# Kernel tuning notes

Measured on AMD Instinct MI355X. Metric: run time of the kernel, lower is better.

Reference implementation:

```python
import jax, jax.numpy as jnp
import numpy as np

N = 100000      # num_nodes
E = 1600000     # num_edges (avg degree 16)
D_IN = 128
D_H = 128
D_OUT = 128


def setup_inputs() -> dict:
    key = jax.random.key(0)
    ks = jax.random.split(key, 6)
    x = jax.random.normal(ks[0], (N, D_IN), dtype=jnp.float32)
    edge_index = jax.random.randint(ks[1], (2, E), 0, N, dtype=jnp.int32)
    s_in = 1.0 / np.sqrt(D_IN)
    s_h = 1.0 / np.sqrt(D_H)
    # nn.Linear weights have shape [out_features, in_features]
    w_neigh1 = jax.random.uniform(ks[2], (D_H, D_IN), jnp.float32, -s_in, s_in)
    w_root1 = jax.random.uniform(ks[3], (D_H, D_IN), jnp.float32, -s_in, s_in)
    w_neigh2 = jax.random.uniform(ks[4], (D_OUT, D_H), jnp.float32, -s_h, s_h)
    w_root2 = jax.random.uniform(ks[5], (D_OUT, D_H), jnp.float32, -s_h, s_h)
    return {
        "x": x,
        "w_neigh1": w_neigh1,
        "w_root1": w_root1,
        "w_neigh2": w_neigh2,
        "w_root2": w_root2,
        "edge_index": edge_index,
    }


def reference(x, w_neigh1, w_root1, w_neigh2, w_root2, edge_index):
    row = edge_index[0]  # destination (row of adjacency)
    col = edge_index[1]  # source / neighbor (column of adjacency)
    # row-normalized adjacency: adj[row, col] = 1 / deg(row)
    deg = jax.ops.segment_sum(jnp.ones(E, x.dtype), row, num_segments=N)
    inv_deg = jnp.where(deg > 0, 1.0 / jnp.maximum(deg, 1.0), 0.0)  # [N]

    def mean_agg(h):
        # spmm: gather neighbor feats [E, d], scatter-add to rows, normalize
        return jax.ops.segment_sum(h[col], row, num_segments=N) * inv_deg[:, None]

    # layer 0: relu(adj @ x @ Wn1^T + x @ Wr1^T)
    h = jax.nn.relu(mean_agg(x) @ w_neigh1.T + x @ w_root1.T)
    # layer 1: adj @ h @ Wn2^T + h @ Wr2^T
    return mean_agg(h) @ w_neigh2.T + h @ w_root2.T
```

## Files before the change

kernel.cpp:

```cpp
#include <hip/hip_runtime.h>

#define NBUK_MAX 2048
#define BNODE 64
#define SORT_CAP 1536
#define AGG_NODES 16
#define AGG_CAP 768
#define SUPER_SHIFT 11
#define NSUPER_MAX 64
#define SUB_PER_SUPER 32

#define QSCALE (127.0f / 6.0f)
#define DEQ (6.0f / 127.0f)

typedef __attribute__((ext_vector_type(8))) short bf16x8;
typedef __attribute__((ext_vector_type(4))) float f32x4;

static __device__ __forceinline__ unsigned int f2bf(float f) {
  unsigned int t = __builtin_bit_cast(unsigned int, f);
  t += 0x7fff + ((t >> 16) & 1);
  return t >> 16;
}
static __device__ __forceinline__ unsigned char f2q(float v) {
  float q = rintf(v * QSCALE);
  q = fminf(fmaxf(q, -127.f), 127.f);
  return (unsigned char)(signed char)(int)q;
}
static __device__ __forceinline__ int sb(unsigned int u, int k) {
  return (int)((signed char)(u >> (k * 8)));
}


__global__ __launch_bounds__(256) void prep_kernel(
    const float* __restrict__ x, unsigned short* __restrict__ Xb,
    unsigned char* __restrict__ Xq, const int* __restrict__ row,
    int* __restrict__ bcount, const float* __restrict__ wn1,
    const float* __restrict__ wr1, const float* __restrict__ wn2,
    const float* __restrict__ wr2, unsigned short* __restrict__ Wp, int N, int E,
    int nbuk, int cvtB) {
  __shared__ int h[NBUK_MAX];
  const int b = blockIdx.x;
  const int tid = threadIdx.x;
  if (b < cvtB) {
    int i = b * 256 + tid;
    int n4 = N * 32;
    if (i < n4) {
      float4 v = ((const float4*)x)[i];
      ushort4 ob;
      ob.x = (unsigned short)f2bf(v.x);
      ob.y = (unsigned short)f2bf(v.y);
      ob.z = (unsigned short)f2bf(v.z);
      ob.w = (unsigned short)f2bf(v.w);
      ((ushort4*)Xb)[i] = ob;
      unsigned int oq = (unsigned)f2q(v.x) | ((unsigned)f2q(v.y) << 8) |
                        ((unsigned)f2q(v.z) << 16) | ((unsigned)f2q(v.w) << 24);
      ((unsigned int*)Xq)[i] = oq;
    }
  } else if (b < cvtB + 256) {
    for (int i = tid; i < nbuk; i += 256) h[i] = 0;
    __syncthreads();
    int hb = b - cvtB;
    for (int e = hb * 256 + tid; e < E; e += 256 * 256)
      atomicAdd(&h[row[e] >> 6], 1);
    __syncthreads();
    for (int i = tid; i < nbuk; i += 256)
      if (h[i]) atomicAdd(&bcount[i], h[i]);
  } else {
    int i = (b - cvtB - 256) * 256 + tid;
    int layer = i >> 15;
    int r = i & 32767;
    int ks = r >> 12;
    int nf = (r >> 9) & 7;
    int lane = (r >> 3) & 63;
    int j = r & 7;
    const float* src = layer ? ((ks < 4) ? wn2 : wr2) : ((ks < 4) ? wn1 : wr1);
    int m = lane & 15, kgrp = lane >> 4;
    int kk = (ks & 3) * 32 + kgrp * 8 + j;
    int n = nf * 16 + m;
    Wp[i] = (unsigned short)f2bf(src[n * 128 + kk]);
  }
}


__global__ __launch_bounds__(1024) void bucket_scan_kernel(
    const int* __restrict__ bcount, int* __restrict__ boff,
    int* __restrict__ bfill, int* __restrict__ sfill, int nbuk, int nsuper,
    int E) {
  __shared__ int s[1024];
  int carry = 0;
  int t = threadIdx.x;
  for (int base = 0; base < nbuk; base += 1024) {
    int v = (base + t < nbuk) ? bcount[base + t] : 0;
    s[t] = v;
    __syncthreads();
    for (int off = 1; off < 1024; off <<= 1) {
      int u = (t >= off) ? s[t - off] : 0;
      __syncthreads();
      s[t] += u;
      __syncthreads();
    }
    if (base + t < nbuk) {
      int ex = carry + s[t] - v;
      boff[base + t] = ex;
      bfill[base + t] = ex;
    }
    carry += s[1023];
    __syncthreads();
  }
  if (t == 0) boff[nbuk] = E;
  __syncthreads();
  if (t < nsuper) {
    int b = t * SUB_PER_SUPER;
    sfill[t] = boff[b > nbuk ? nbuk : b];
  }
}


__global__ __launch_bounds__(256) void s1_scatter(
    const int* __restrict__ row, const int* __restrict__ col,
    int* __restrict__ sfill, int* __restrict__ sbuf, int E) {
  __shared__ int cnt[NSUPER_MAX];
  __shared__ int base[NSUPER_MAX];
  int per = (E + gridDim.x - 1) / gridDim.x;
  int e0 = blockIdx.x * per;
  int e1 = e0 + per;
  if (e1 > E) e1 = E;
  if (threadIdx.x < NSUPER_MAX) cnt[threadIdx.x] = 0;
  __syncthreads();
  for (int e = e0 + threadIdx.x; e < e1; e += 256)
    atomicAdd(&cnt[row[e] >> SUPER_SHIFT], 1);
  __syncthreads();
  if (threadIdx.x < NSUPER_MAX) {
    int c = cnt[threadIdx.x];
    base[threadIdx.x] = c ? atomicAdd(&sfill[threadIdx.x], c) : 0;
    cnt[threadIdx.x] = 0;
  }
  __syncthreads();
  for (int e = e0 + threadIdx.x; e < e1; e += 256) {
    int r = row[e];
    int sp = r >> SUPER_SHIFT;
    int rk = atomicAdd(&cnt[sp], 1);
    sbuf[base[sp] + rk] = ((r & ((1 << SUPER_SHIFT) - 1)) << 17) | col[e];
  }
}


__global__ __launch_bounds__(256) void s2_scatter(
    const int* __restrict__ boff, const int* __restrict__ sbuf,
    int* __restrict__ bfill, int* __restrict__ bbuf, int nbuk) {
  __shared__ int cnt[SUB_PER_SUPER];
  __shared__ int base[SUB_PER_SUPER];
  const int sp = blockIdx.x >> 4;
  const int bp = blockIdx.x & 15;
  const int b0 = sp * SUB_PER_SUPER;
  int bend = b0 + SUB_PER_SUPER;
  if (bend > nbuk) bend = nbuk;
  const int sstart = boff[b0];
  const int len = boff[bend] - sstart;
  const int i0 = sstart + (len * bp) / 16;
  const int i1 = sstart + (len * (bp + 1)) / 16;
  if (threadIdx.x < SUB_PER_SUPER) cnt[threadIdx.x] = 0;
  __syncthreads();
  for (int i = i0 + threadIdx.x; i < i1; i += 256)
    atomicAdd(&cnt[(((unsigned)sbuf[i]) >> 17) >> 6], 1);
  __syncthreads();
  if (threadIdx.x < SUB_PER_SUPER) {
    int c = cnt[threadIdx.x];
    base[threadIdx.x] = c ? atomicAdd(&bfill[b0 + threadIdx.x], c) : 0;
    cnt[threadIdx.x] = 0;
  }
  __syncthreads();
  for (int i = i0 + threadIdx.x; i < i1; i += 256) {
    int p = sbuf[i];
    unsigned rl = ((unsigned)p) >> 17;
    int sub = rl >> 6;
    int rk = atomicAdd(&cnt[sub], 1);
    bbuf[base[sub] + rk] = ((rl & 63) << 17) | (p & 0x1FFFF);
  }
}


__global__ __launch_bounds__(256) void p2_sort_kernel(
    const int* __restrict__ boff, int* __restrict__ bbuf,
    int* __restrict__ rowptr, int* __restrict__ ovf, int N, int E) {
  __shared__ int cols[SORT_CAP];
  __shared__ int hist[BNODE], startc[BNODE], fillc[BNODE];
  const int b = blockIdx.x;
  const int tid = threadIdx.x;
  const int gs = boff[b], ge = boff[b + 1];
  const int bsize = ge - gs;
  if (tid < BNODE) hist[tid] = 0;
  __syncthreads();
  for (int i = gs + tid; i < ge; i += 256)
    atomicAdd(&hist[((unsigned)bbuf[i]) >> 17], 1);
  __syncthreads();
  if (tid < 64) {
    int v = hist[tid];
    int s = v;
    #pragma unroll
    for (int off = 1; off < 64; off <<= 1) {
      int u = __shfl_up(s, off, 64);
      if (tid >= off) s += u;
    }
    startc[tid] = s - v;
    fillc[tid] = s - v;
  }
  __syncthreads();
  const bool fast = (bsize <= SORT_CAP);
  if (fast) {
    for (int i = tid; i < bsize; i += 256) {
      int p = bbuf[gs + i];
      int k = atomicAdd(&fillc[((unsigned)p) >> 17], 1);
      cols[k] = p & 0x1FFFF;
    }
  }
  __syncthreads();
  if (fast) {
    for (int i = tid; i < bsize; i += 256) bbuf[gs + i] = cols[i];
  } else if (tid == 0) {
    ovf[b] = 1;
  }
  if (tid < BNODE) {
    int node = b * BNODE + tid;
    if (node < N) rowptr[node] = gs + startc[tid];
  }
  if (b == 0 && tid == 0) rowptr[N] = E;
}


__global__ __launch_bounds__(256) void agg_i8_kernel(
    const unsigned char* __restrict__ qtab, const int* __restrict__ rowptr,
    const int* __restrict__ bbuf, const int* __restrict__ boff,
    const int* __restrict__ ovf, unsigned short* __restrict__ out, int N) {
  __shared__ int cols[AGG_CAP];
  __shared__ int rp[AGG_NODES + 1];
  const int tid = threadIdx.x;
  const int n0 = blockIdx.x * AGG_NODES;
  if (tid <= AGG_NODES) {
    int nn = n0 + tid;
    rp[tid] = rowptr[nn > N ? N : nn];
  }
  __syncthreads();
  const int e0 = rp[0];
  const int range = rp[AGG_NODES] - e0;
  const int buck = n0 >> 6;
  const bool bovf = (ovf[buck] != 0);
  const bool lds = (!bovf) && (range <= AGG_CAP);
  if (lds) {
    for (int i = tid; i < range; i += 256) cols[i] = bbuf[e0 + i];
  }
  __syncthreads();

  const int g = tid >> 4;
  const int fl = tid & 15;
  const int node = n0 + g;
  if (node >= N) return;
  const int d = rp[g + 1] - rp[g];
  const char* fb = (const char*)qtab;
  const unsigned foff = (unsigned)fl * 8;
  int a[8];
  #pragma unroll
  for (int j = 0; j < 8; ++j) a[j] = 0;

  if (!bovf) {
    const int* cp = lds ? (cols + (rp[g] - e0)) : (bbuf + rp[g]);
    int k = 0;
    for (; k + 8 <= d; k += 8) {
      unsigned o[8];
      #pragma unroll
      for (int j = 0; j < 8; ++j) o[j] = ((unsigned)cp[k + j] << 7) + foff;
      uint2 v[8];
      #pragma unroll
      for (int j = 0; j < 8; ++j) v[j] = *(const uint2*)(fb + o[j]);
      #pragma unroll
      for (int j = 0; j < 8; ++j) {
        a[0] += sb(v[j].x, 0);
        a[1] += sb(v[j].x, 1);
        a[2] += sb(v[j].x, 2);
        a[3] += sb(v[j].x, 3);
        a[4] += sb(v[j].y, 0);
        a[5] += sb(v[j].y, 1);
        a[6] += sb(v[j].y, 2);
        a[7] += sb(v[j].y, 3);
      }
    }
    for (; k < d; ++k) {
      uint2 v = *(const uint2*)(fb + (((unsigned)cp[k] << 7) + foff));
      a[0] += sb(v.x, 0);
      a[1] += sb(v.x, 1);
      a[2] += sb(v.x, 2);
      a[3] += sb(v.x, 3);
      a[4] += sb(v.y, 0);
      a[5] += sb(v.y, 1);
      a[6] += sb(v.y, 2);
      a[7] += sb(v.y, 3);
    }
  } else {
    int gsb = boff[buck], geb = boff[buck + 1];
    unsigned int nl = (unsigned)(node & (BNODE - 1));
    for (int i = gsb; i < geb; ++i) {
      int p = bbuf[i];
      if ((((unsigned)p) >> 17) == nl) {
        uint2 v = *(const uint2*)(fb + (((unsigned)(p & 0x1FFFF) << 7) + foff));
        a[0] += sb(v.x, 0);
        a[1] += sb(v.x, 1);
        a[2] += sb(v.x, 2);
        a[3] += sb(v.x, 3);
        a[4] += sb(v.y, 0);
        a[5] += sb(v.y, 1);
        a[6] += sb(v.y, 2);
        a[7] += sb(v.y, 3);
      }
    }
  }

  float m = ((d > 0) ? 1.0f / (float)d : 0.f) * DEQ;
  uint4 pk;
  pk.x = f2bf((float)a[0] * m) | (f2bf((float)a[1] * m) << 16);
  pk.y = f2bf((float)a[2] * m) | (f2bf((float)a[3] * m) << 16);
  pk.z = f2bf((float)a[4] * m) | (f2bf((float)a[5] * m) << 16);
  pk.w = f2bf((float)a[6] * m) | (f2bf((float)a[7] * m) << 16);
  *(uint4*)((char*)out + ((unsigned)node << 8) + (unsigned)fl * 16) = pk;
}


template <bool RELU, bool OUT_BF16, bool EMIT_I8>
__global__ __launch_bounds__(256) void mfma_gemm_kernel(
    const unsigned short* __restrict__ Aagg,
    const unsigned short* __restrict__ Aroot,
    const unsigned short* __restrict__ Wpack,
    void* __restrict__ Cout, unsigned char* __restrict__ Qout, int nrows) {
  const int lane = threadIdx.x & 63;
  const int wid = threadIdx.x >> 6;
  const int row0 = blockIdx.x * 64 + wid * 16;
  const int m = lane & 15;
  const int kgrp = lane >> 4;
  int arow = row0 + m;
  if (arow > nrows - 1) arow = nrows - 1;

  bf16x8 a[8];
  #pragma unroll
  for (int ks = 0; ks < 4; ++ks)
    a[ks] = *(const bf16x8*)(Aagg + (size_t)arow * 128 + ks * 32 + kgrp * 8);
  #pragma unroll
  for (int ks = 4; ks < 8; ++ks)
    a[ks] = *(const bf16x8*)(Aroot + (size_t)arow * 128 + (ks - 4) * 32 + kgrp * 8);

  f32x4 acc[8];
  #pragma unroll
  for (int i = 0; i < 8; ++i) acc[i] = (f32x4){0.f, 0.f, 0.f, 0.f};

  const unsigned short* wp = Wpack + (size_t)lane * 8;
  #pragma unroll
  for (int ks = 0; ks < 8; ++ks) {
    #pragma unroll
    for (int nf = 0; nf < 8; ++nf) {
      bf16x8 bfr = *(const bf16x8*)(wp + ((ks * 8 + nf) << 9));
      acc[nf] = __builtin_amdgcn_mfma_f32_16x16x32_bf16(a[ks], bfr, acc[nf], 0, 0, 0);
    }
  }

  const int crow0 = row0 + kgrp * 4;
  #pragma unroll
  for (int nf = 0; nf < 8; ++nf) {
    int c = nf * 16 + m;
    #pragma unroll
    for (int j = 0; j < 4; ++j) {
      int r = crow0 + j;
      if (r < nrows) {
        float v = acc[nf][j];
        if (RELU) v = fmaxf(v, 0.f);
        if (OUT_BF16)
          ((unsigned short*)Cout)[(size_t)r * 128 + c] = (unsigned short)f2bf(v);
        else
          ((float*)Cout)[(size_t)r * 128 + c] = v;
        if (EMIT_I8) Qout[(size_t)r * 128 + c] = f2q(v);
      }
    }
  }
}


extern "C" void kernel_launch(void* const* d_in, const int* in_sizes, int n_in,
                              void* d_out, int out_size, void* d_ws, size_t ws_size,
                              hipStream_t stream) {
  const float* x = (const float*)d_in[0];
  const float* wn1 = (const float*)d_in[1];
  const float* wr1 = (const float*)d_in[2];
  const float* wn2 = (const float*)d_in[3];
  const float* wr2 = (const float*)d_in[4];
  const int* ei = (const int*)d_in[5];
  const int N = in_sizes[0] / 128;
  const int E = in_sizes[5] / 2;
  const int* row = ei;
  const int* col = ei + E;
  const int NBUK = (N + BNODE - 1) / BNODE;
  const int NSUPER = (N + (1 << SUPER_SHIFT) - 1) >> SUPER_SHIFT;

  char* p = (char*)d_ws;
  unsigned short* Xb = (unsigned short*)p;  p += (size_t)N * 128 * 2;
  unsigned short* Hb = (unsigned short*)p;  p += (size_t)N * 128 * 2;
  int* bbuf = (int*)p;      p += (size_t)E * 4;
  int* sbuf = (int*)p;      p += (size_t)E * 4;
  int* rowptr = (int*)p;    p += (size_t)(N + 1) * 4;
  int* bcount = (int*)p;    p += NBUK_MAX * 4;
  int* ovf = (int*)p;       p += NBUK_MAX * 4;
  int* boff = (int*)p;      p += (NBUK_MAX + 1) * 4;
  int* bfill = (int*)p;     p += NBUK_MAX * 4;
  int* sfill = (int*)p;     p += NSUPER_MAX * 4;
  unsigned short* Wp = (unsigned short*)p;  p += 2 * 32768 * 2;
  unsigned short* Wp1 = Wp;
  unsigned short* Wp2 = Wp + 32768;

  unsigned short* agg1 = (unsigned short*)d_out;
  unsigned char* Xq = (unsigned char*)d_out + (size_t)N * 128 * 2;
  unsigned char* Hq = (unsigned char*)d_out + (size_t)N * 128 * 3;
  unsigned short* agg2 = Xb;

  hipMemsetAsync(bcount, 0, 2 * NBUK_MAX * 4, stream);
  int cvtB = (N * 32 + 255) / 256;
  prep_kernel<<<cvtB + 512, 256, 0, stream>>>(x, Xb, Xq, row, bcount, wn1, wr1,
                                              wn2, wr2, Wp, N, E, NBUK, cvtB);

  bucket_scan_kernel<<<1, 1024, 0, stream>>>(bcount, boff, bfill, sfill, NBUK,
                                             NSUPER, E);
  s1_scatter<<<512, 256, 0, stream>>>(row, col, sfill, sbuf, E);
  s2_scatter<<<NSUPER * 16, 256, 0, stream>>>(boff, sbuf, bfill, bbuf, NBUK);
  p2_sort_kernel<<<NBUK, 256, 0, stream>>>(boff, bbuf, rowptr, ovf, N, E);

  agg_i8_kernel<<<(N + AGG_NODES - 1) / AGG_NODES, 256, 0, stream>>>(
      Xq, rowptr, bbuf, boff, ovf, agg1, N);
  mfma_gemm_kernel<true, true, true><<<(N + 63) / 64, 256, 0, stream>>>(
      agg1, Xb, Wp1, Hb, Hq, N);

  agg_i8_kernel<<<(N + AGG_NODES - 1) / AGG_NODES, 256, 0, stream>>>(
      Hq, rowptr, bbuf, boff, ovf, agg2, N);
  mfma_gemm_kernel<false, false, false><<<(N + 63) / 64, 256, 0, stream>>>(
      agg2, Hb, Wp2, (void*)d_out, nullptr, N);
}
```

Before: 204.5 us.

## Fuse int8 neighbor aggregation with MFMA GEMM per 64-node bucket

Each layer now runs as one kernel. A block aggregates the int8 neighbor features for a 64-node bucket into an LDS tile, then runs the bf16 MFMA projection directly from that tile, so the aggregated matrix is never written to or read back from global memory. Layer 1 converts fp32 x to bf16 on the fly in the GEMM, which drops the separate bf16 copy of x from the prep kernel. The cost is fewer, heavier blocks in which each thread gathers for four nodes in sequence, so there is less parallelism to hide gather latency.

```diff
diff --git a/kernel.cpp b/kernel.cpp
--- a/kernel.cpp
+++ b/kernel.cpp
@@ -3,8 +3,6 @@
 #define NBUK_MAX 2048
 #define BNODE 64
 #define SORT_CAP 1536
-#define AGG_NODES 16
-#define AGG_CAP 768
 #define SUPER_SHIFT 11
 #define NSUPER_MAX 64
 #define SUB_PER_SUPER 32
@@ -31,12 +29,11 @@
 
 
 __global__ __launch_bounds__(256) void prep_kernel(
-    const float* __restrict__ x, unsigned short* __restrict__ Xb,
-    unsigned char* __restrict__ Xq, const int* __restrict__ row,
-    int* __restrict__ bcount, const float* __restrict__ wn1,
-    const float* __restrict__ wr1, const float* __restrict__ wn2,
-    const float* __restrict__ wr2, unsigned short* __restrict__ Wp, int N, int E,
-    int nbuk, int cvtB) {
+    const float* __restrict__ x, unsigned char* __restrict__ Xq,
+    const int* __restrict__ row, int* __restrict__ bcount,
+    const float* __restrict__ wn1, const float* __restrict__ wr1,
+    const float* __restrict__ wn2, const float* __restrict__ wr2,
+    unsigned short* __restrict__ Wp, int N, int E, int nbuk, int cvtB) {
   __shared__ int h[NBUK_MAX];
   const int b = blockIdx.x;
   const int tid = threadIdx.x;
@@ -45,12 +42,6 @@
     int n4 = N * 32;
     if (i < n4) {
       float4 v = ((const float4*)x)[i];
-      ushort4 ob;
-      ob.x = (unsigned short)f2bf(v.x);
-      ob.y = (unsigned short)f2bf(v.y);
-      ob.z = (unsigned short)f2bf(v.z);
-      ob.w = (unsigned short)f2bf(v.w);
-      ((ushort4*)Xb)[i] = ob;
       unsigned int oq = (unsigned)f2q(v.x) | ((unsigned)f2q(v.y) << 8) |
                         ((unsigned)f2q(v.z) << 16) | ((unsigned)f2q(v.w) << 24);
       ((unsigned int*)Xq)[i] = oq;
@@ -227,128 +218,152 @@
 }
 
 
-__global__ __launch_bounds__(256) void agg_i8_kernel(
-    const unsigned char* __restrict__ qtab, const int* __restrict__ rowptr,
-    const int* __restrict__ bbuf, const int* __restrict__ boff,
-    const int* __restrict__ ovf, unsigned short* __restrict__ out, int N) {
-  __shared__ int cols[AGG_CAP];
-  __shared__ int rp[AGG_NODES + 1];
+template <bool L1>
+__global__ __launch_bounds__(256) void fused_kernel(
+    const unsigned char* __restrict__ qtab,
+    const void* __restrict__ root,
+    const unsigned short* __restrict__ Wpack,
+    const int* __restrict__ rowptr, const int* __restrict__ bbuf,
+    const int* __restrict__ ovf, void* __restrict__ Cout,
+    unsigned char* __restrict__ Qout, int nrows) {
+  __shared__ short aggL[BNODE][132];
+  __shared__ int cols[SORT_CAP];
+  __shared__ int rp[BNODE + 1];
   const int tid = threadIdx.x;
-  const int n0 = blockIdx.x * AGG_NODES;
-  if (tid <= AGG_NODES) {
+  const int b = blockIdx.x;
+  const int n0 = b * BNODE;
+
+  if (tid <= BNODE) {
     int nn = n0 + tid;
-    rp[tid] = rowptr[nn > N ? N : nn];
-  }
-  __syncthreads();
-  const int e0 = rp[0];
-  const int range = rp[AGG_NODES] - e0;
-  const int buck = n0 >> 6;
-  const bool bovf = (ovf[buck] != 0);
-  const bool lds = (!bovf) && (range <= AGG_CAP);
-  if (lds) {
-    for (int i = tid; i < range; i += 256) cols[i] = bbuf[e0 + i];
-  }
-  __syncthreads();
-
-  const int g = tid >> 4;
-  const int fl = tid & 15;
-  const int node = n0 + g;
-  if (node >= N) return;
-  const int d = rp[g + 1] - rp[g];
-  const char* fb = (const char*)qtab;
-  const unsigned foff = (unsigned)fl * 8;
-  int a[8];
-  #pragma unroll
-  for (int j = 0; j < 8; ++j) a[j] = 0;
-
+    rp[tid] = rowptr[nn > nrows ? nrows : nn];
+  }
+  __syncthreads();
+  const int gs = rp[0];
+  const int bsize = rp[BNODE] - gs;
+  const bool bovf = (ovf[b] != 0);
   if (!bovf) {
-    const int* cp = lds ? (cols + (rp[g] - e0)) : (bbuf + rp[g]);
-    int k = 0;
-    for (; k + 8 <= d; k += 8) {
-      unsigned o[8];
+    for (int i = tid; i < bsize; i += 256) cols[i] = bbuf[gs + i];
+  }
+  __syncthreads();
+
+  {
+    const int g = tid >> 4;
+    const int fl = tid & 15;
+    const char* fb = (const char*)qtab;
+    const unsigned foff = (unsigned)fl * 8;
+    for (int q = 0; q < 4; ++q) {
+      const int nl = (g << 2) + q;
+      const int node = n0 + nl;
+      if (node >= nrows) continue;
+      const int d = rp[nl + 1] - rp[nl];
+      int a[8];
       #pragma unroll
-      for (int j = 0; j < 8; ++j) o[j] = ((unsigned)cp[k + j] << 7) + foff;
-      uint2 v[8];
-      #pragma unroll
-      for (int j = 0; j < 8; ++j) v[j] = *(const uint2*)(fb + o[j]);
-      #pragma unroll
-      for (int j = 0; j < 8; ++j) {
-        a[0] += sb(v[j].x, 0);
-        a[1] += sb(v[j].x, 1);
-        a[2] += sb(v[j].x, 2);
-        a[3] += sb(v[j].x, 3);
-        a[4] += sb(v[j].y, 0);
-        a[5] += sb(v[j].y, 1);
-        a[6] += sb(v[j].y, 2);
-        a[7] += sb(v[j].y, 3);
+      for (int j = 0; j < 8; ++j) a[j] = 0;
+      if (!bovf) {
+        const int* cp = cols + (rp[nl] - gs);
+        int k = 0;
+        for (; k + 8 <= d; k += 8) {
+          unsigned o[8];
+          #pragma unroll
+          for (int j = 0; j < 8; ++j) o[j] = ((unsigned)cp[k + j] << 7) + foff;
+          uint2 v[8];
+          #pragma unroll
+          for (int j = 0; j < 8; ++j) v[j] = *(const uint2*)(fb + o[j]);
+          #pragma unroll
+          for (int j = 0; j < 8; ++j) {
+            a[0] += sb(v[j].x, 0);
+            a[1] += sb(v[j].x, 1);
+            a[2] += sb(v[j].x, 2);
+            a[3] += sb(v[j].x, 3);
+            a[4] += sb(v[j].y, 0);
+            a[5] += sb(v[j].y, 1);
+            a[6] += sb(v[j].y, 2);
+            a[7] += sb(v[j].y, 3);
+          }
+        }
+        for (; k < d; ++k) {
+          uint2 v = *(const uint2*)(fb + (((unsigned)cp[k] << 7) + foff));
+          a[0] += sb(v.x, 0);
+          a[1] += sb(v.x, 1);
+          a[2] += sb(v.x, 2);
+          a[3] += sb(v.x, 3);
+          a[4] += sb(v.y, 0);
+          a[5] += sb(v.y, 1);
+          a[6] += sb(v.y, 2);
+          a[7] += sb(v.y, 3);
+        }
+      } else {
+        unsigned int nl_u = (unsigned)nl;
+        for (int i = 0; i < bsize; ++i) {
+          int p = bbuf[gs + i];
+          if ((((unsigned)p) >> 17) == nl_u) {
+            uint2 v = *(const uint2*)(fb + (((unsigned)(p & 0x1FFFF) << 7) + foff));
+            a[0] += sb(v.x, 0);
+            a[1] += sb(v.x, 1);
+            a[2] += sb(v.x, 2);
+            a[3] += sb(v.x, 3);
+            a[4] += sb(v.y, 0);
+            a[5] += sb(v.y, 1);
+            a[6] += sb(v.y, 2);
+            a[7] += sb(v.y, 3);
+          }
+        }
       }
-    }
-    for (; k < d; ++k) {
-      uint2 v = *(const uint2*)(fb + (((unsigned)cp[k] << 7) + foff));
-      a[0] += sb(v.x, 0);
-      a[1] += sb(v.x, 1);
-      a[2] += sb(v.x, 2);
-      a[3] += sb(v.x, 3);
-      a[4] += sb(v.y, 0);
-      a[5] += sb(v.y, 1);
-      a[6] += sb(v.y, 2);
-      a[7] += sb(v.y, 3);
-    }
-  } else {
-    int gsb = boff[buck], geb = boff[buck + 1];
-    unsigned int nl = (unsigned)(node & (BNODE - 1));
-    for (int i = gsb; i < geb; ++i) {
-      int p = bbuf[i];
-      if ((((unsigned)p) >> 17) == nl) {
-        uint2 v = *(const uint2*)(fb + (((unsigned)(p & 0x1FFFF) << 7) + foff));
-        a[0] += sb(v.x, 0);
-        a[1] += sb(v.x, 1);
-        a[2] += sb(v.x, 2);
-        a[3] += sb(v.x, 3);
-        a[4] += sb(v.y, 0);
-        a[5] += sb(v.y, 1);
-        a[6] += sb(v.y, 2);
-        a[7] += sb(v.y, 3);
-      }
-    }
-  }
-
-  float m = ((d > 0) ? 1.0f / (float)d : 0.f) * DEQ;
-  uint4 pk;
-  pk.x = f2bf((float)a[0] * m) | (f2bf((float)a[1] * m) << 16);
-  pk.y = f2bf((float)a[2] * m) | (f2bf((float)a[3] * m) << 16);
-  pk.z = f2bf((float)a[4] * m) | (f2bf((float)a[5] * m) << 16);
-  pk.w = f2bf((float)a[6] * m) | (f2bf((float)a[7] * m) << 16);
-  *(uint4*)((char*)out + ((unsigned)node << 8) + (unsigned)fl * 16) = pk;
-}
-
-
-template <bool RELU, bool OUT_BF16, bool EMIT_I8>
-__global__ __launch_bounds__(256) void mfma_gemm_kernel(
-    const unsigned short* __restrict__ Aagg,
-    const unsigned short* __restrict__ Aroot,
-    const unsigned short* __restrict__ Wpack,
-    void* __restrict__ Cout, unsigned char* __restrict__ Qout, int nrows) {
-  const int lane = threadIdx.x & 63;
-  const int wid = threadIdx.x >> 6;
-  const int row0 = blockIdx.x * 64 + wid * 16;
+      float m = ((d > 0) ? 1.0f / (float)d : 0.f) * DEQ;
+      unsigned p0 = f2bf((float)a[0] * m) | (f2bf((float)a[1] * m) << 16);
+      unsigned p1 = f2bf((float)a[2] * m) | (f2bf((float)a[3] * m) << 16);
+      unsigned p2 = f2bf((float)a[4] * m) | (f2bf((float)a[5] * m) << 16);
+      unsigned p3 = f2bf((float)a[6] * m) | (f2bf((float)a[7] * m) << 16);
+      short* dst = &aggL[nl][fl * 8];
+      *(uint2*)dst = make_uint2(p0, p1);
+      *(uint2*)(dst + 4) = make_uint2(p2, p3);
+    }
+  }
+  __syncthreads();
+
+  const int lane = tid & 63;
+  const int wid = tid >> 6;
   const int m = lane & 15;
   const int kgrp = lane >> 4;
-  int arow = row0 + m;
-  if (arow > nrows - 1) arow = nrows - 1;
+  int lr = (wid << 4) + m;
+  if (n0 + lr > nrows - 1) lr = nrows - 1 - n0;
+  const int arow = n0 + lr;
 
   bf16x8 a[8];
   #pragma unroll
-  for (int ks = 0; ks < 4; ++ks)
-    a[ks] = *(const bf16x8*)(Aagg + (size_t)arow * 128 + ks * 32 + kgrp * 8);
-  #pragma unroll
-  for (int ks = 4; ks < 8; ++ks)
-    a[ks] = *(const bf16x8*)(Aroot + (size_t)arow * 128 + (ks - 4) * 32 + kgrp * 8);
+  for (int ks = 0; ks < 4; ++ks) {
+    const short* ap = &aggL[lr][ks * 32 + kgrp * 8];
+    ((uint2*)&a[ks])[0] = *(const uint2*)ap;
+    ((uint2*)&a[ks])[1] = *(const uint2*)(ap + 4);
+  }
+  if (L1) {
+    const float* xf = (const float*)root;
+    #pragma unroll
+    for (int ks = 4; ks < 8; ++ks) {
+      const float* sp = xf + (size_t)arow * 128 + (ks - 4) * 32 + kgrp * 8;
+      float4 v0 = *(const float4*)sp;
+      float4 v1 = *(const float4*)(sp + 4);
+      bf16x8 t;
+      t[0] = (short)f2bf(v0.x);
+      t[1] = (short)f2bf(v0.y);
+      t[2] = (short)f2bf(v0.z);
+      t[3] = (short)f2bf(v0.w);
+      t[4] = (short)f2bf(v1.x);
+      t[5] = (short)f2bf(v1.y);
+      t[6] = (short)f2bf(v1.z);
+      t[7] = (short)f2bf(v1.w);
+      a[ks] = t;
+    }
+  } else {
+    const unsigned short* hb = (const unsigned short*)root;
+    #pragma unroll
+    for (int ks = 4; ks < 8; ++ks)
+      a[ks] = *(const bf16x8*)(hb + (size_t)arow * 128 + (ks - 4) * 32 + kgrp * 8);
+  }
 
   f32x4 acc[8];
   #pragma unroll
   for (int i = 0; i < 8; ++i) acc[i] = (f32x4){0.f, 0.f, 0.f, 0.f};
-
   const unsigned short* wp = Wpack + (size_t)lane * 8;
   #pragma unroll
   for (int ks = 0; ks < 8; ++ks) {
@@ -359,7 +374,7 @@
     }
   }
 
-  const int crow0 = row0 + kgrp * 4;
+  const int crow0 = n0 + (wid << 4) + kgrp * 4;
   #pragma unroll
   for (int nf = 0; nf < 8; ++nf) {
     int c = nf * 16 + m;
@@ -368,12 +383,13 @@
       int r = crow0 + j;
       if (r < nrows) {
         float v = acc[nf][j];
-        if (RELU) v = fmaxf(v, 0.f);
-        if (OUT_BF16)
+        if (L1) {
+          v = fmaxf(v, 0.f);
           ((unsigned short*)Cout)[(size_t)r * 128 + c] = (unsigned short)f2bf(v);
-        else
+          Qout[(size_t)r * 128 + c] = f2q(v);
+        } else {
           ((float*)Cout)[(size_t)r * 128 + c] = v;
-        if (EMIT_I8) Qout[(size_t)r * 128 + c] = f2q(v);
+        }
       }
     }
   }
@@ -397,8 +413,8 @@
   const int NSUPER = (N + (1 << SUPER_SHIFT) - 1) >> SUPER_SHIFT;
 
   char* p = (char*)d_ws;
-  unsigned short* Xb = (unsigned short*)p;  p += (size_t)N * 128 * 2;
   unsigned short* Hb = (unsigned short*)p;  p += (size_t)N * 128 * 2;
+  unsigned char* Hq = (unsigned char*)p;    p += (size_t)N * 128;
   int* bbuf = (int*)p;      p += (size_t)E * 4;
   int* sbuf = (int*)p;      p += (size_t)E * 4;
   int* rowptr = (int*)p;    p += (size_t)(N + 1) * 4;
@@ -411,15 +427,12 @@
   unsigned short* Wp1 = Wp;
   unsigned short* Wp2 = Wp + 32768;
 
-  unsigned short* agg1 = (unsigned short*)d_out;
-  unsigned char* Xq = (unsigned char*)d_out + (size_t)N * 128 * 2;
-  unsigned char* Hq = (unsigned char*)d_out + (size_t)N * 128 * 3;
-  unsigned short* agg2 = Xb;
+  unsigned char* Xq = (unsigned char*)d_out;
 
   hipMemsetAsync(bcount, 0, 2 * NBUK_MAX * 4, stream);
   int cvtB = (N * 32 + 255) / 256;
-  prep_kernel<<<cvtB + 512, 256, 0, stream>>>(x, Xb, Xq, row, bcount, wn1, wr1,
-                                              wn2, wr2, Wp, N, E, NBUK, cvtB);
+  prep_kernel<<<cvtB + 512, 256, 0, stream>>>(x, Xq, row, bcount, wn1, wr1, wn2,
+                                              wr2, Wp, N, E, NBUK, cvtB);
 
   bucket_scan_kernel<<<1, 1024, 0, stream>>>(bcount, boff, bfill, sfill, NBUK,
                                              NSUPER, E);
@@ -427,13 +440,9 @@
   s2_scatter<<<NSUPER * 16, 256, 0, stream>>>(boff, sbuf, bfill, bbuf, NBUK);
   p2_sort_kernel<<<NBUK, 256, 0, stream>>>(boff, bbuf, rowptr, ovf, N, E);
 
-  agg_i8_kernel<<<(N + AGG_NODES - 1) / AGG_NODES, 256, 0, stream>>>(
-      Xq, rowptr, bbuf, boff, ovf, agg1, N);
-  mfma_gemm_kernel<true, true, true><<<(N + 63) / 64, 256, 0, stream>>>(
-      agg1, Xb, Wp1, Hb, Hq, N);
-
-  agg_i8_kernel<<<(N + AGG_NODES - 1) / AGG_NODES, 256, 0, stream>>>(
-      Hq, rowptr, bbuf, boff, ovf, agg2, N);
-  mfma_gemm_kernel<false, false, false><<<(N + 63) / 64, 256, 0, stream>>>(
-      agg2, Hb, Wp2, (void*)d_out, nullptr, N);
-}
+  fused_kernel<true><<<NBUK, 256, 0, stream>>>(Xq, x, Wp1, rowptr, bbuf, ovf,
+                                               Hb, Hq, N);
+
+  fused_kernel<false><<<NBUK, 256, 0, stream>>>(Hq, Hb, Wp2, rowptr, bbuf, ovf,
+                                                (void*)d_out, nullptr, N);
+}
```

Measured after the change: 215.1 us. +5.2%, slower.
